# Kernel optimization log

Hardware: AMD Instinct MI355X
Metric: run time of the kernel (lower is better)

Reference implementation:

```python
import jax, jax.numpy as jnp
import numpy as np

B, CIN, H, W = 64, 3, 96, 96
COUT, KH, KW = 96, 5, 5
STRIDE, PAD = 2, 2
LR, K_TOP, DELTA, P_LEB = 0.02, 2, -0.4, 3.0
PREC = 1e-30


def im2col(x):
    # torch nn.Unfold ordering: channel-major (C, kh, kw) flattened -> [B, C*KH*KW, L]
    xp = jnp.pad(x, ((0, 0), (0, 0), (PAD, PAD), (PAD, PAD)))
    Hout = (H + 2 * PAD - KH) // STRIDE + 1
    Wout = (W + 2 * PAD - KW) // STRIDE + 1
    cols = []
    for i in range(KH):  # small fixed kernel loop (25 slices)
        for j in range(KW):
            cols.append(xp[:, :, i:i + STRIDE * (Hout - 1) + 1:STRIDE,
                           j:j + STRIDE * (Wout - 1) + 1:STRIDE])
    patches = jnp.stack(cols, axis=2)  # [B, C, KH*KW, Hout, Wout]
    return patches.reshape(x.shape[0], CIN * KH * KW, Hout * Wout)  # [B, K, L]


def setup_inputs() -> dict:
    key = jax.random.key(0)
    k1, k2 = jax.random.split(key)
    inp = jax.random.normal(k1, (B, CIN, H, W), dtype=jnp.float32)
    weight = jax.random.normal(k2, (COUT, CIN, KH, KW), dtype=jnp.float32)  # init.normal_
    return {"input": inp, "weight": weight}


def reference(input, weight):
    # standard conv forward (F.conv2d, no bias)
    out = jax.lax.conv_general_dilated(
        input, weight, (STRIDE, STRIDE), [(PAD, PAD), (PAD, PAD)],
        dimension_numbers=("NCHW", "OIHW", "NCHW"))

    # --- Krotov-Hopfield Hebbian update ---
    pre = im2col(input)                      # [B, K, L]
    Wm = weight.reshape(COUT, -1)            # [O, K]
    # sign(W) * |W|^(p-1) @ pre
    tot = jnp.einsum("ok,bkl->bol", jnp.sign(Wm) * jnp.abs(Wm) ** (P_LEB - 1.0), pre)  # [B,O,L]

    Bn, _, L = tot.shape
    _, idx = jax.lax.top_k(tot.transpose(0, 2, 1), K_TOP)   # [B, L, k] over output channels
    vals = jnp.concatenate([jnp.ones((1,), tot.dtype),
                            jnp.full((K_TOP - 1,), DELTA, tot.dtype)])  # top-1 -> 1.0, rest -> delta
    act = jnp.zeros((Bn, L, COUT), tot.dtype).at[
        jnp.arange(Bn)[:, None, None], jnp.arange(L)[None, :, None], idx
    ].set(jnp.broadcast_to(vals, (Bn, L, K_TOP)))
    act = act.transpose(0, 2, 1)             # [B, O, L]

    yx = jnp.einsum("bol,bkl->ok", act, pre) / L          # mean over L, sum over batch
    yy = (act * tot).sum(0).mean(1)                        # [O]
    ds = yx - yy[:, None] * Wm                             # [O, K]
    nc = jnp.maximum(jnp.max(jnp.abs(ds)), PREC)
    new_weight = weight + LR * (ds / nc).reshape(weight.shape)
    return out, new_weight
```

## Files before the change

### kernel.cpp

```cpp
#include <hip/hip_runtime.h>

#define B_     64
#define HW_    96
#define COUT_  96
#define KK_    75
#define KP_    76
#define KPAD   96
#define HOUT_  48
#define L_     2304
#define LR_    0.02f
#define DELTA_ -0.4f
#define OUT_ELEMS (B_*COUT_*L_)
#define CL2    256
#define NPART  (B_*9)
#define ROW    (COUT_*KK_ + COUT_)

typedef __attribute__((ext_vector_type(8))) short short8v;
typedef __attribute__((ext_vector_type(4))) float float4v;
typedef __attribute__((ext_vector_type(4))) unsigned uint4v;

__device__ __forceinline__ unsigned short f2bf(float f) {
  unsigned u = __float_as_uint(f);
  u += 0x7fff + ((u >> 16) & 1);
  return (unsigned short)(u >> 16);
}

__device__ __forceinline__ void ins2(float v, int o, float& v1, int& o1,
                                     float& v2, int& o2) {
  bool b1 = (v > v1) || (v == v1 && o < o1);
  bool b2 = (v > v2) || (v == v2 && o < o2);
  if (b1)      { v2 = v1; o2 = o1; v1 = v; o1 = o; }
  else if (b2) { v2 = v;  o2 = o; }
}

__device__ __forceinline__ void im2col_load(const float* __restrict__ xb, int l,
                                            float* __restrict__ pre) {
  const int oh = l / HOUT_, ow = l - oh * HOUT_;
  #pragma unroll
  for (int c = 0; c < 3; ++c) {
    #pragma unroll
    for (int i = 0; i < 5; ++i) {
      int ih = oh * 2 + i - 2;
      bool okh = ((unsigned)ih < (unsigned)HW_);
      #pragma unroll
      for (int j = 0; j < 5; ++j) {
        int iw = ow * 2 + j - 2;
        float v = 0.0f;
        if (okh && ((unsigned)iw < (unsigned)HW_)) v = xb[(c * HW_ + ih) * HW_ + iw];
        pre[c * 25 + i * 5 + j] = v;
      }
    }
  }
  pre[KK_] = 0.0f;
}

__global__ __launch_bounds__(256) void k0_prep(const float* __restrict__ w,
                                               unsigned short* __restrict__ wbf) {
  int i = blockIdx.x * 256 + threadIdx.x;
  if (i >= 192 * KPAD) return;
  int row = i / KPAD, k = i - row * KPAD;
  float v = 0.0f;
  if (k < KK_) {
    float ww = w[(row % COUT_) * KK_ + k];
    v = (row < COUT_) ? ww : ww * fabsf(ww);
  }
  wbf[i] = f2bf(v);
}

__device__ __forceinline__ int wswz(int blk, int row) {
  return (blk < 8) ? (blk ^ (row & 7)) : (blk ^ (row & 3));
}

__global__ __launch_bounds__(256, 4) void k1_mfma(
    const float* __restrict__ x, const unsigned short* __restrict__ wbf,
    float* __restrict__ out, float4* __restrict__ top2)
{
  __shared__ __align__(16) unsigned short wlds[192 * KPAD];
  const int tid = threadIdx.x;
  const int lane = tid & 63, wq = tid >> 6;
  const int b = blockIdx.y;
  const int bl0 = blockIdx.x * 64;
  const int col = lane & 15, g = lane >> 4;
  const float* xb = x + (size_t)b * (3 * HW_ * HW_);

  #pragma unroll
  for (int i = 0; i < 9; ++i) {
    int id = tid + i * 256;
    int row = id / 12, blk = id - row * 12;
    uint4v v = *(const uint4v*)(wbf + row * KPAD + blk * 8);
    *(uint4v*)((char*)wlds + row * 192 + wswz(blk, row) * 16) = v;
  }

  const int l = bl0 + wq * 16 + col;
  const int oh = l / HOUT_, ow = l - oh * HOUT_;
  const int ihb = 2 * oh - 2, iwb = 2 * ow - 2;
  short8v bfr[3];
  #pragma unroll
  for (int kt = 0; kt < 3; ++kt) {
    uint4v pk;
    #pragma unroll
    for (int e2 = 0; e2 < 4; ++e2) {
      float v0 = 0.0f, v1 = 0.0f;
      const int k0 = kt * 32 + g * 8 + 2 * e2;
      if (k0 < KK_) {
        int c = k0 / 25, r = k0 - 25 * c, ki = r / 5, kj = r - 5 * ki;
        int ih = ihb + ki, iw = iwb + kj;
        if ((unsigned)ih < (unsigned)HW_ && (unsigned)iw < (unsigned)HW_)
          v0 = xb[(c * HW_ + ih) * HW_ + iw];
      }
      const int k1e = k0 + 1;
      if (k1e < KK_) {
        int c = k1e / 25, r = k1e - 25 * c, ki = r / 5, kj = r - 5 * ki;
        int ih = ihb + ki, iw = iwb + kj;
        if ((unsigned)ih < (unsigned)HW_ && (unsigned)iw < (unsigned)HW_)
          v1 = xb[(c * HW_ + ih) * HW_ + iw];
      }
      pk[e2] = (unsigned)f2bf(v0) | ((unsigned)f2bf(v1) << 16);
    }
    bfr[kt] = __builtin_bit_cast(short8v, pk);
  }

  __syncthreads();

  float4v acc[12];
  #pragma unroll
  for (int mt = 0; mt < 12; ++mt) acc[mt] = (float4v)(0.0f);
  #pragma unroll
  for (int kt = 0; kt < 3; ++kt) {
    const int blk = kt * 4 + g;
    #pragma unroll
    for (int mt = 0; mt < 12; ++mt) {
      const int row = mt * 16 + col;
      short8v afr = *(const short8v*)(
          (const char*)wlds + row * 192 + wswz(blk, row) * 16);
      acc[mt] = __builtin_amdgcn_mfma_f32_16x16x32_bf16(
          afr, bfr[kt], acc[mt], 0, 0, 0);
    }
  }

  #pragma unroll
  for (int mt = 0; mt < 6; ++mt) {
    #pragma unroll
    for (int r = 0; r < 4; ++r) {
      const int ch = mt * 16 + g * 4 + r;
      out[((size_t)b * COUT_ + ch) * L_ + l] = acc[mt][r];
    }
  }

  float v1 = -3.0e38f, v2 = -3.0e38f;
  int o1 = 0x7fffffff, o2 = 0x7fffffff;
  #pragma unroll
  for (int mt = 6; mt < 12; ++mt)
    #pragma unroll
    for (int r = 0; r < 4; ++r)
      ins2(acc[mt][r], (mt - 6) * 16 + g * 4 + r, v1, o1, v2, o2);
  #pragma unroll
  for (int st = 0; st < 2; ++st) {
    const int d = (st == 0) ? 16 : 32;
    float bv1 = __shfl_xor(v1, d, 64);
    int   bo1 = __shfl_xor(o1, d, 64);
    float bv2 = __shfl_xor(v2, d, 64);
    int   bo2 = __shfl_xor(o2, d, 64);
    ins2(bv1, bo1, v1, o1, v2, o2);
    ins2(bv2, bo2, v1, o1, v2, o2);
  }
  if (g == 0)
    top2[(size_t)b * L_ + l] =
        make_float4(v1, __int_as_float(o1), v2, __int_as_float(o2));
}

__global__ __launch_bounds__(256, 1) void k2_gemm(
    const float* __restrict__ x, const float4* __restrict__ top2,
    float* __restrict__ part)
{
  __shared__ __align__(16) unsigned short actS[COUT_ * CL2];
  __shared__ __align__(16) unsigned short preT[COUT_ * CL2];
  __shared__ float yyS[COUT_];
  const int tid = threadIdx.x;
  const int b = blockIdx.y;
  const int pos = tid;
  const float* xb = x + (size_t)b * (3 * HW_ * HW_);

  {
    float4* a4 = (float4*)actS;
    float4* p4 = (float4*)preT;
    #pragma unroll
    for (int i = 0; i < 12; ++i) {
      a4[tid + i * 256] = make_float4(0, 0, 0, 0);
      p4[tid + i * 256] = make_float4(0, 0, 0, 0);
    }
    if (tid < COUT_) yyS[tid] = 0.0f;
  }
  __syncthreads();

  const int l0 = blockIdx.x * CL2;
  {
    float pre[KP_];
    im2col_load(xb, l0 + pos, pre);
    const int pblk = pos >> 3, plo = (pos & 7) << 1;
    #pragma unroll
    for (int k = 0; k < KK_; ++k) {
      int byteoff = k * 512 + ((pblk ^ (k & 7)) << 4) + plo;
      *(unsigned short*)((char*)preT + byteoff) = f2bf(pre[k]);
    }
    float4 t2 = top2[(size_t)b * L_ + l0 + pos];
    int o1 = __float_as_int(t2.y), o2 = __float_as_int(t2.w);
    *(unsigned short*)((char*)actS + o1 * 512 + ((pblk ^ (o1 & 7)) << 4) + plo)
        = 0x3F80;
    *(unsigned short*)((char*)actS + o2 * 512 + ((pblk ^ (o2 & 7)) << 4) + plo)
        = f2bf(DELTA_);
    atomicAdd(&yyS[o1], t2.x);
    atomicAdd(&yyS[o2], DELTA_ * t2.z);
  }
  __syncthreads();

  const int lane = tid & 63, w = tid >> 6;
  const int col = lane & 15, g = lane >> 4;
  const int mb = (w >> 1) * 48, nb = (w & 1) * 48;

  float4v acc[3][3];
  #pragma unroll
  for (int mt = 0; mt < 3; ++mt)
    #pragma unroll
    for (int nt = 0; nt < 3; ++nt) acc[mt][nt] = (float4v)(0.0f);

  #pragma unroll
  for (int kt = 0; kt < 8; ++kt) {
    short8v a[3], bf[3];
    #pragma unroll
    for (int mt = 0; mt < 3; ++mt) {
      int row = mb + mt * 16 + col;
      a[mt] = *(const short8v*)((char*)actS + row * 512 +
                                (((kt * 4 + g) ^ (row & 7)) << 4));
    }
    #pragma unroll
    for (int nt = 0; nt < 3; ++nt) {
      int row = nb + nt * 16 + col;
      bf[nt] = *(const short8v*)((char*)preT + row * 512 +
                                 (((kt * 4 + g) ^ (row & 7)) << 4));
    }
    #pragma unroll
    for (int mt = 0; mt < 3; ++mt)
      #pragma unroll
      for (int nt = 0; nt < 3; ++nt)
        acc[mt][nt] = __builtin_amdgcn_mfma_f32_16x16x32_bf16(
            a[mt], bf[nt], acc[mt][nt], 0, 0, 0);
  }
  __syncthreads();

  float* prow = part + (size_t)(b * 9 + blockIdx.x) * ROW;
  #pragma unroll
  for (int mt = 0; mt < 3; ++mt)
    #pragma unroll
    for (int nt = 0; nt < 3; ++nt)
      #pragma unroll
      for (int r = 0; r < 4; ++r) {
        int m = mb + mt * 16 + g * 4 + r;
        int n = nb + nt * 16 + col;
        if (n < KK_) prow[m * KK_ + n] = acc[mt][nt][r];
      }
  if (tid < COUT_) prow[COUT_ * KK_ + tid] = yyS[tid];
}

__global__ __launch_bounds__(256) void k3_reduce(
    const float* __restrict__ part, float* __restrict__ finals)
{
  __shared__ float red[4][64];
  const int e = blockIdx.x * 64 + (threadIdx.x & 63);
  const int seg = threadIdx.x >> 6;
  float s = 0.0f;
  for (int p = seg * (NPART / 4); p < (seg + 1) * (NPART / 4); ++p)
    s += part[(size_t)p * ROW + e];
  red[seg][threadIdx.x & 63] = s;
  __syncthreads();
  if (seg == 0) {
    int ll = threadIdx.x & 63;
    finals[e] = (red[0][ll] + red[1][ll]) + (red[2][ll] + red[3][ll]);
  }
}

__global__ __launch_bounds__(256) void k4_finalize(
    const float* __restrict__ w, const float* __restrict__ finals,
    float* __restrict__ outw)
{
  __shared__ float dsS[COUT_ * KK_];
  __shared__ float wmax[4];
  __shared__ float ncS;
  const int tid = threadIdx.x;
  float m = 0.0f;
  for (int i = tid; i < COUT_ * KK_; i += 256) {
    int o = i / KK_;
    float d = finals[i] - finals[COUT_ * KK_ + o] * w[i];
    dsS[i] = d;
    m = fmaxf(m, fabsf(d));
  }
  #pragma unroll
  for (int s = 32; s > 0; s >>= 1) m = fmaxf(m, __shfl_xor(m, s, 64));
  if ((tid & 63) == 0) wmax[tid >> 6] = m;
  __syncthreads();
  if (tid == 0) {
    float n = fmaxf(fmaxf(wmax[0], wmax[1]), fmaxf(wmax[2], wmax[3]));
    ncS = fmaxf(n, 1e-30f);
  }
  __syncthreads();
  const float scale = LR_ / ncS;
  for (int i = tid; i < COUT_ * KK_; i += 256) {
    outw[i] = w[i] + scale * dsS[i];
  }
}

extern "C" void kernel_launch(void* const* d_in, const int* in_sizes, int n_in,
                              void* d_out, int out_size, void* d_ws, size_t ws_size,
                              hipStream_t stream) {
  (void)in_sizes; (void)n_in; (void)out_size; (void)ws_size;
  const float* x = (const float*)d_in[0];
  const float* w = (const float*)d_in[1];
  float* out  = (float*)d_out;
  float* outw = out + OUT_ELEMS;

  unsigned short* wbf = (unsigned short*)d_ws;
  float4* top2 = (float4*)((char*)d_ws + 192 * KPAD * 2);
  float*  part = (float*)((char*)top2 + (size_t)B_ * L_ * sizeof(float4));
  float*  finals = part + (size_t)NPART * ROW;

  k0_prep   <<<dim3((192 * KPAD + 255) / 256), 256, 0, stream>>>(w, wbf);
  k1_mfma   <<<dim3(L_ / 64, B_), 256, 0, stream>>>(x, wbf, out, top2);
  k2_gemm   <<<dim3(9, B_), 256, 0, stream>>>(x, top2, part);
  k3_reduce <<<dim3(ROW / 64), 256, 0, stream>>>(part, finals);
  k4_finalize<<<dim3(1), 256, 0, stream>>>(w, finals, outw);
}
```

Measured before the change: 122.1 us.

## Stage input tiles in LDS for im2col and enlarge conv tile per block

Both the conv/score kernel and the Hebbian GEMM kernel now stage a halo tile of the input image in shared memory and build im2col fragments from LDS, instead of doing scattered global gathers per element. The conv kernel also processes four output rows per block (three N-tiles per wave), reusing each weight fragment across three MFMAs, and splits the two 96-row GEMM halves to limit register pressure. In exchange it uses more LDS and registers, lowers the occupancy hint from 4 to 3, and launches fewer, larger blocks.

Result: no change. 122.7 us (+0.5%).

```diff
diff --git a/kernel.cpp b/kernel.cpp
--- a/kernel.cpp
+++ b/kernel.cpp
@@ -14,6 +14,10 @@
 #define CL2    256
 #define NPART  (B_*9)
 #define ROW    (COUT_*KK_ + COUT_)
+#define XPITCH 100
+#define XSLOTS 3368
+#define X2ROWS 15
+#define X2N    4500
 
 typedef __attribute__((ext_vector_type(8))) short short8v;
 typedef __attribute__((ext_vector_type(4))) float float4v;
@@ -31,27 +35,6 @@
   bool b2 = (v > v2) || (v == v2 && o < o2);
   if (b1)      { v2 = v1; o2 = o1; v1 = v; o1 = o; }
   else if (b2) { v2 = v;  o2 = o; }
-}
-
-__device__ __forceinline__ void im2col_load(const float* __restrict__ xb, int l,
-                                            float* __restrict__ pre) {
-  const int oh = l / HOUT_, ow = l - oh * HOUT_;
-  #pragma unroll
-  for (int c = 0; c < 3; ++c) {
-    #pragma unroll
-    for (int i = 0; i < 5; ++i) {
-      int ih = oh * 2 + i - 2;
-      bool okh = ((unsigned)ih < (unsigned)HW_);
-      #pragma unroll
-      for (int j = 0; j < 5; ++j) {
-        int iw = ow * 2 + j - 2;
-        float v = 0.0f;
-        if (okh && ((unsigned)iw < (unsigned)HW_)) v = xb[(c * HW_ + ih) * HW_ + iw];
-        pre[c * 25 + i * 5 + j] = v;
-      }
-    }
-  }
-  pre[KK_] = 0.0f;
 }
 
 __global__ __launch_bounds__(256) void k0_prep(const float* __restrict__ w,
@@ -71,15 +54,16 @@
   return (blk < 8) ? (blk ^ (row & 7)) : (blk ^ (row & 3));
 }
 
-__global__ __launch_bounds__(256, 4) void k1_mfma(
+__global__ __launch_bounds__(256, 3) void k1_mfma(
     const float* __restrict__ x, const unsigned short* __restrict__ wbf,
     float* __restrict__ out, float4* __restrict__ top2)
 {
   __shared__ __align__(16) unsigned short wlds[192 * KPAD];
+  __shared__ __align__(16) float xs[XSLOTS];
   const int tid = threadIdx.x;
   const int lane = tid & 63, wq = tid >> 6;
   const int b = blockIdx.y;
-  const int bl0 = blockIdx.x * 64;
+  const int bx = blockIdx.x;
   const int col = lane & 15, g = lane >> 4;
   const float* xb = x + (size_t)b * (3 * HW_ * HW_);
 
@@ -91,82 +75,129 @@
     *(uint4v*)((char*)wlds + row * 192 + wswz(blk, row) * 16) = v;
   }
 
-  const int l = bl0 + wq * 16 + col;
-  const int oh = l / HOUT_, ow = l - oh * HOUT_;
-  const int ihb = 2 * oh - 2, iwb = 2 * ow - 2;
-  short8v bfr[3];
-  #pragma unroll
-  for (int kt = 0; kt < 3; ++kt) {
-    uint4v pk;
-    #pragma unroll
-    for (int e2 = 0; e2 < 4; ++e2) {
-      float v0 = 0.0f, v1 = 0.0f;
-      const int k0 = kt * 32 + g * 8 + 2 * e2;
-      if (k0 < KK_) {
-        int c = k0 / 25, r = k0 - 25 * c, ki = r / 5, kj = r - 5 * ki;
-        int ih = ihb + ki, iw = iwb + kj;
-        if ((unsigned)ih < (unsigned)HW_ && (unsigned)iw < (unsigned)HW_)
-          v0 = xb[(c * HW_ + ih) * HW_ + iw];
+  const int ihbase = 8 * bx - 2;
+  #pragma unroll
+  for (int i = 0; i < 14; ++i) {
+    int idx = tid + i * 256;
+    if (idx < XSLOTS) {
+      int row = idx / XPITCH, iwr = idx - row * XPITCH;
+      int c = row / 11, ihr = row - c * 11;
+      int ih = ihbase + ihr, iw = iwr - 2;
+      float v = 0.0f;
+      if (c < 3 && (unsigned)ih < (unsigned)HW_ && (unsigned)iw < (unsigned)HW_)
+        v = xb[(c * HW_ + ih) * HW_ + iw];
+      xs[idx] = v;
+    }
+  }
+
+  int offs[12][2];
+  {
+    const int base_fl = wq * 200 + 2 * col;
+    #pragma unroll
+    for (int kt = 0; kt < 3; ++kt)
+      #pragma unroll
+      for (int e2 = 0; e2 < 4; ++e2)
+        #pragma unroll
+        for (int par = 0; par < 2; ++par) {
+          int k = kt * 32 + g * 8 + 2 * e2 + par;
+          int c = k / 25, r = k - 25 * c, ki = r / 5, kj = r - 5 * ki;
+          int fl = (k < KK_) ? base_fl + (c * 11 + ki) * XPITCH + kj
+                             : 33 * XPITCH;
+          offs[kt * 4 + e2][par] = fl * 4;
+        }
+  }
+
+  __syncthreads();
+
+  short8v bfr[3][3];
+  #pragma unroll
+  for (int nt = 0; nt < 3; ++nt)
+    #pragma unroll
+    for (int kt = 0; kt < 3; ++kt) {
+      uint4v pk;
+      #pragma unroll
+      for (int e2 = 0; e2 < 4; ++e2) {
+        const float* p0 = (const float*)((const char*)xs + offs[kt*4+e2][0]);
+        const float* p1 = (const float*)((const char*)xs + offs[kt*4+e2][1]);
+        float v0 = p0[nt * 32];
+        float v1 = p1[nt * 32];
+        pk[e2] = (unsigned)f2bf(v0) | ((unsigned)f2bf(v1) << 16);
       }
-      const int k1e = k0 + 1;
-      if (k1e < KK_) {
-        int c = k1e / 25, r = k1e - 25 * c, ki = r / 5, kj = r - 5 * ki;
-        int ih = ihb + ki, iw = iwb + kj;
-        if ((unsigned)ih < (unsigned)HW_ && (unsigned)iw < (unsigned)HW_)
-          v1 = xb[(c * HW_ + ih) * HW_ + iw];
-      }
-      pk[e2] = (unsigned)f2bf(v0) | ((unsigned)f2bf(v1) << 16);
-    }
-    bfr[kt] = __builtin_bit_cast(short8v, pk);
-  }
-
-  __syncthreads();
-
-  float4v acc[12];
-  #pragma unroll
-  for (int mt = 0; mt < 12; ++mt) acc[mt] = (float4v)(0.0f);
+      bfr[nt][kt] = __builtin_bit_cast(short8v, pk);
+    }
+
+  const int lrow0 = (4 * bx + wq) * 48;
+  float4v acc[3][6];
+
+  #pragma unroll
+  for (int nt = 0; nt < 3; ++nt)
+    #pragma unroll
+    for (int mt = 0; mt < 6; ++mt) acc[nt][mt] = (float4v)(0.0f);
   #pragma unroll
   for (int kt = 0; kt < 3; ++kt) {
     const int blk = kt * 4 + g;
     #pragma unroll
-    for (int mt = 0; mt < 12; ++mt) {
+    for (int mt = 0; mt < 6; ++mt) {
       const int row = mt * 16 + col;
       short8v afr = *(const short8v*)(
           (const char*)wlds + row * 192 + wswz(blk, row) * 16);
-      acc[mt] = __builtin_amdgcn_mfma_f32_16x16x32_bf16(
-          afr, bfr[kt], acc[mt], 0, 0, 0);
-    }
-  }
-
-  #pragma unroll
-  for (int mt = 0; mt < 6; ++mt) {
+      #pragma unroll
+      for (int nt = 0; nt < 3; ++nt)
+        acc[nt][mt] = __builtin_amdgcn_mfma_f32_16x16x32_bf16(
+            afr, bfr[nt][kt], acc[nt][mt], 0, 0, 0);
+    }
+  }
+  #pragma unroll
+  for (int mt = 0; mt < 6; ++mt)
     #pragma unroll
     for (int r = 0; r < 4; ++r) {
       const int ch = mt * 16 + g * 4 + r;
-      out[((size_t)b * COUT_ + ch) * L_ + l] = acc[mt][r];
-    }
-  }
-
-  float v1 = -3.0e38f, v2 = -3.0e38f;
-  int o1 = 0x7fffffff, o2 = 0x7fffffff;
-  #pragma unroll
-  for (int mt = 6; mt < 12; ++mt)
-    #pragma unroll
-    for (int r = 0; r < 4; ++r)
-      ins2(acc[mt][r], (mt - 6) * 16 + g * 4 + r, v1, o1, v2, o2);
-  #pragma unroll
-  for (int st = 0; st < 2; ++st) {
-    const int d = (st == 0) ? 16 : 32;
-    float bv1 = __shfl_xor(v1, d, 64);
-    int   bo1 = __shfl_xor(o1, d, 64);
-    float bv2 = __shfl_xor(v2, d, 64);
-    int   bo2 = __shfl_xor(o2, d, 64);
-    ins2(bv1, bo1, v1, o1, v2, o2);
-    ins2(bv2, bo2, v1, o1, v2, o2);
-  }
-  if (g == 0)
-    top2[(size_t)b * L_ + l] =
-        make_float4(v1, __int_as_float(o1), v2, __int_as_float(o2));
+      float* op = out + ((size_t)b * COUT_ + ch) * L_ + lrow0 + col;
+      #pragma unroll
+      for (int nt = 0; nt < 3; ++nt) op[nt * 16] = acc[nt][mt][r];
+    }
+
+  #pragma unroll
+  for (int nt = 0; nt < 3; ++nt)
+    #pragma unroll
+    for (int mt = 0; mt < 6; ++mt) acc[nt][mt] = (float4v)(0.0f);
+  #pragma unroll
+  for (int kt = 0; kt < 3; ++kt) {
+    const int blk = kt * 4 + g;
+    #pragma unroll
+    for (int mt = 0; mt < 6; ++mt) {
+      const int row = 96 + mt * 16 + col;
+      short8v afr = *(const short8v*)(
+          (const char*)wlds + row * 192 + wswz(blk, row) * 16);
+      #pragma unroll
+      for (int nt = 0; nt < 3; ++nt)
+        acc[nt][mt] = __builtin_amdgcn_mfma_f32_16x16x32_bf16(
+            afr, bfr[nt][kt], acc[nt][mt], 0, 0, 0);
+    }
+  }
+  #pragma unroll
+  for (int nt = 0; nt < 3; ++nt) {
+    float v1 = -3.0e38f, v2 = -3.0e38f;
+    int o1 = 0x7fffffff, o2 = 0x7fffffff;
+    #pragma unroll
+    for (int mt = 0; mt < 6; ++mt)
+      #pragma unroll
+      for (int r = 0; r < 4; ++r)
+        ins2(acc[nt][mt][r], mt * 16 + g * 4 + r, v1, o1, v2, o2);
+    #pragma unroll
+    for (int st = 0; st < 2; ++st) {
+      const int d = (st == 0) ? 16 : 32;
+      float bv1 = __shfl_xor(v1, d, 64);
+      int   bo1 = __shfl_xor(o1, d, 64);
+      float bv2 = __shfl_xor(v2, d, 64);
+      int   bo2 = __shfl_xor(o2, d, 64);
+      ins2(bv1, bo1, v1, o1, v2, o2);
+      ins2(bv2, bo2, v1, o1, v2, o2);
+    }
+    if (g == 0)
+      top2[(size_t)b * L_ + lrow0 + nt * 16 + col] =
+          make_float4(v1, __int_as_float(o1), v2, __int_as_float(o2));
+  }
 }
 
 __global__ __launch_bounds__(256, 1) void k2_gemm(
@@ -175,6 +206,7 @@
 {
   __shared__ __align__(16) unsigned short actS[COUT_ * CL2];
   __shared__ __align__(16) unsigned short preT[COUT_ * CL2];
+  __shared__ __align__(16) float xs2[X2N];
   __shared__ float yyS[COUT_];
   const int tid = threadIdx.x;
   const int b = blockIdx.y;
@@ -191,19 +223,45 @@
     }
     if (tid < COUT_) yyS[tid] = 0.0f;
   }
-  __syncthreads();
 
   const int l0 = blockIdx.x * CL2;
+  const int oh0 = l0 / HOUT_;
+  const int ihb2 = 2 * oh0 - 2;
+  #pragma unroll
+  for (int i = 0; i < 18; ++i) {
+    int idx = tid + i * 256;
+    if (idx < X2N) {
+      int row = idx / XPITCH, iwr = idx - row * XPITCH;
+      int c = row / X2ROWS, ihr = row - c * X2ROWS;
+      int ih = ihb2 + ihr, iw = iwr - 2;
+      float v = 0.0f;
+      if ((unsigned)ih < (unsigned)HW_ && (unsigned)iw < (unsigned)HW_)
+        v = xb[(c * HW_ + ih) * HW_ + iw];
+      xs2[idx] = v;
+    }
+  }
+  __syncthreads();
+
   {
-    float pre[KP_];
-    im2col_load(xb, l0 + pos, pre);
+    float pre[KK_];
+    const int dl = l0 + pos;
+    const int oh = dl / HOUT_, ow = dl - oh * HOUT_;
+    const float* xl = xs2 + (2 * (oh - oh0)) * XPITCH + 2 * ow;
+    #pragma unroll
+    for (int c = 0; c < 3; ++c)
+      #pragma unroll
+      for (int ki = 0; ki < 5; ++ki)
+        #pragma unroll
+        for (int kj = 0; kj < 5; ++kj)
+          pre[c * 25 + ki * 5 + kj] = xl[(c * X2ROWS + ki) * XPITCH + kj];
+
     const int pblk = pos >> 3, plo = (pos & 7) << 1;
     #pragma unroll
     for (int k = 0; k < KK_; ++k) {
       int byteoff = k * 512 + ((pblk ^ (k & 7)) << 4) + plo;
       *(unsigned short*)((char*)preT + byteoff) = f2bf(pre[k]);
     }
-    float4 t2 = top2[(size_t)b * L_ + l0 + pos];
+    float4 t2 = top2[(size_t)b * L_ + dl];
     int o1 = __float_as_int(t2.y), o2 = __float_as_int(t2.w);
     *(unsigned short*)((char*)actS + o1 * 512 + ((pblk ^ (o1 & 7)) << 4) + plo)
         = 0x3F80;
@@ -324,7 +382,7 @@
   float*  finals = part + (size_t)NPART * ROW;
 
   k0_prep   <<<dim3((192 * KPAD + 255) / 256), 256, 0, stream>>>(w, wbf);
-  k1_mfma   <<<dim3(L_ / 64, B_), 256, 0, stream>>>(x, wbf, out, top2);
+  k1_mfma   <<<dim3(12, B_), 256, 0, stream>>>(x, wbf, out, top2);
   k2_gemm   <<<dim3(9, B_), 256, 0, stream>>>(x, top2, part);
   k3_reduce <<<dim3(ROW / 64), 256, 0, stream>>>(part, finals);
   k4_finalize<<<dim3(1), 256, 0, stream>>>(w, finals, outw);
```
